# Kernel tuning notes

Measured on AMD Instinct MI355X. Metric: run time of the kernel, lower is better.

## Reference

```python
import jax, jax.numpy as jnp
import numpy as np

B, G, D, N_HEADS, FFN, L = 16, 2048, 256, 8, 1024, 4
HEAD_DIM = D // N_HEADS
EPS_LN = 1e-5
MASK_TOKEN = -10.0
REE_BASE = 100.0


def setup_inputs() -> dict:
    key = jax.random.key(0)
    ks = jax.random.split(key, 20)
    s = 0.02
    inp = {
        'x': jax.random.normal(ks[0], (B, G), jnp.float32),
        'gene_emb': jax.random.normal(ks[1], (G, D), jnp.float32) * s,
        'inv_freq': (1.0 / REE_BASE ** (jnp.arange(0, D, 2, dtype=jnp.float32) / D)),
        'Wq': jax.random.normal(ks[2], (L, D, D), jnp.float32) * s,
        'bq': jnp.zeros((L, D), jnp.float32),
        'Wk': jax.random.normal(ks[3], (L, D, D), jnp.float32) * s,
        'bk': jnp.zeros((L, D), jnp.float32),
        'Wv': jax.random.normal(ks[4], (L, D, D), jnp.float32) * s,
        'bv': jnp.zeros((L, D), jnp.float32),
        'ln1_g': jnp.ones((L, D), jnp.float32),
        'ln1_b': jnp.zeros((L, D), jnp.float32),
        'ln2_g': jnp.ones((L, D), jnp.float32),
        'ln2_b': jnp.zeros((L, D), jnp.float32),
        'WU': jax.random.normal(ks[5], (L, D, FFN), jnp.float32) * s,
        'bU': jnp.zeros((L, FFN), jnp.float32),
        'WV': jax.random.normal(ks[6], (L, FFN, D), jnp.float32) * s,
        'bV': jnp.zeros((L, D), jnp.float32),
        'Wout': jax.random.normal(ks[7], (D, 1), jnp.float32) * s,
        'bout': jnp.zeros((1,), jnp.float32),
    }
    return inp


def layernorm(x, g, b):
    m = x.mean(-1, keepdims=True)
    v = ((x - m) ** 2).mean(-1, keepdims=True)
    return (x - m) / jnp.sqrt(v + EPS_LN) * g + b


def causal_linear_attention(q, k, v):
    # q, k already feature-mapped ('sqr'); shapes [B, S, H, dh]
    b, s, h, dh = q.shape
    qs, ks_, vs = (jnp.moveaxis(t, 1, 0) for t in (q, k, v))  # [S,B,H,dh]
    num0 = jnp.zeros((b, h, dh, dh), q.dtype)
    den0 = jnp.zeros((b, h, dh), q.dtype)

    def step(carry, qkv):
        num_s, den_s = carry
        qt, kt, vt = qkv
        num_s = num_s + jnp.einsum('bhf,bhd->bhfd', kt, vt)
        den_s = den_s + kt
        num = jnp.einsum('bhf,bhfd->bhd', qt, num_s)
        den = jnp.einsum('bhf,bhf->bh', qt, den_s)
        return (num_s, den_s), num / (den[..., None] + 1e-16)

    _, out = jax.lax.scan(step, (num0, den0), (qs, ks_, vs))  # [S,B,H,dh]
    return jnp.moveaxis(out, 0, 1).reshape(b, s, h * dh)


def reference(x, gene_emb, inv_freq, Wq, bq, Wk, bk, Wv, bv,
              ln1_g, ln1_b, ln2_g, ln2_b, WU, bU, WV, bV, Wout, bout):
    b, g = x.shape
    # Rotary Expression Embedding
    freqs = x[..., None] * inv_freq  # [B,G,D/2]
    emb = jnp.concatenate([jnp.sin(freqs), jnp.cos(freqs)], axis=-1)  # [B,G,D]
    emb = jnp.where((x == MASK_TOKEN)[..., None], 0.0, emb)
    h = gene_emb[None] + emb  # [B,G,D]

    for l in range(Wq.shape[0]):
        hn = layernorm(h, ln1_g[l], ln1_b[l])  # pre-LN (on_gptln=True)
        q = (hn @ Wq[l] + bq[l]).reshape(b, g, N_HEADS, HEAD_DIM) ** 2
        k = (hn @ Wk[l] + bk[l]).reshape(b, g, N_HEADS, HEAD_DIM) ** 2
        v = (hn @ Wv[l] + bv[l]).reshape(b, g, N_HEADS, HEAD_DIM)
        h = h + causal_linear_attention(q, k, v)
        hn2 = layernorm(h, ln2_g[l], ln2_b[l])
        h = h + jax.nn.gelu(hn2 @ WU[l] + bU[l], approximate=False) @ WV[l] + bV[l]
    return (h @ Wout + bout).squeeze(-1)  # [B,G]
```

## Files before the change

kernel.cpp:

```cpp
#include <hip/hip_runtime.h>
#include <math.h>


#define GG 2048
#define DD 256
#define NROWS 32768
#define NC 32
#define CS 64

typedef __attribute__((ext_vector_type(8))) short bf16x8;
typedef __attribute__((ext_vector_type(4))) float f32x4;

__device__ __forceinline__ short f2bf(float f) {
  union { float f; unsigned u; } v; v.f = f;
  unsigned r = v.u + 0x7FFFu + ((v.u >> 16) & 1u);
  return (short)(r >> 16);
}
__device__ __forceinline__ float bf2f(short s) {
  union { unsigned u; float f; } v; v.u = ((unsigned)(unsigned short)s) << 16;
  return v.f;
}
__device__ __forceinline__ void gld16(const short* g, short* l) {
  __builtin_amdgcn_global_load_lds(
      (const __attribute__((address_space(1))) void*)g,
      (__attribute__((address_space(3))) void*)l, 16, 0, 0);
}
__device__ __forceinline__ float fast_gelu(float x) {
  float y = 1.595769122f * (x + 0.044715f * x * x * x);
  return x / (1.0f + __expf(-y));
}

__global__ __launch_bounds__(256) void embed_kernel(
    const float* __restrict__ x, const float* __restrict__ ge,
    const float* __restrict__ invf, float* __restrict__ h) {
  int bg = blockIdx.x * 4 + (threadIdx.x >> 6);
  int g = bg & (GG - 1);
  int lane = threadIdx.x & 63;
  float xv = x[bg];
  int d = lane * 4;
  float4 e;
  if (lane < 32) {
    float4 f = *(const float4*)&invf[d];
    e.x = sinf(xv * f.x); e.y = sinf(xv * f.y);
    e.z = sinf(xv * f.z); e.w = sinf(xv * f.w);
  } else {
    float4 f = *(const float4*)&invf[d - 128];
    e.x = cosf(xv * f.x); e.y = cosf(xv * f.y);
    e.z = cosf(xv * f.z); e.w = cosf(xv * f.w);
  }
  if (xv == -10.0f) { e.x = 0.f; e.y = 0.f; e.z = 0.f; e.w = 0.f; }
  float4 gv = *(const float4*)&ge[(size_t)g * DD + d];
  float4 o; o.x = gv.x + e.x; o.y = gv.y + e.y; o.z = gv.z + e.z; o.w = gv.w + e.w;
  *(float4*)&h[(size_t)bg * DD + d] = o;
}

__global__ __launch_bounds__(256) void ln_tiled(
    const float* __restrict__ h, const float* __restrict__ gamma,
    const float* __restrict__ beta, short* __restrict__ outT) {
  __shared__ float mean_s[32], rstd_s[32];
  __shared__ float gls[256], bls[256];
  int r0 = blockIdx.x * 32;
  int tid = threadIdx.x;
  gls[tid] = gamma[tid]; bls[tid] = beta[tid];
  {
    int row = tid >> 3, seg = tid & 7;
    const float4* hp = (const float4*)(h + (size_t)(r0 + row) * DD + seg * 32);
    float s = 0.f, s2 = 0.f;
#pragma unroll
    for (int i = 0; i < 8; ++i) {
      float4 v = hp[i];
      s += v.x + v.y + v.z + v.w;
      s2 += v.x * v.x + v.y * v.y + v.z * v.z + v.w * v.w;
    }
    s += __shfl_xor(s, 1); s += __shfl_xor(s, 2); s += __shfl_xor(s, 4);
    s2 += __shfl_xor(s2, 1); s2 += __shfl_xor(s2, 2); s2 += __shfl_xor(s2, 4);
    if (seg == 0) {
      float mn = s * (1.0f / 256.0f);
      mean_s[row] = mn;
      rstd_s[row] = rsqrtf(s2 * (1.0f / 256.0f) - mn * mn + 1e-5f);
    }
  }
  __syncthreads();
  int row = tid & 31, kc8 = (tid >> 5) & 3, half = tid >> 7;
  float mn = mean_s[row], rs = rstd_s[row];
  size_t hrow = (size_t)(r0 + row) * DD;
  int trow = (r0 & 127) + row;
  short* tb = outT + (size_t)(r0 >> 7) * 8 * 4096 + (kc8 * 128 + trow) * 8;
#pragma unroll
  for (int j = 0; j < 4; ++j) {
    int kb = half * 4 + j;
    int k0 = kb * 32 + kc8 * 8;
    float4 x0 = *(const float4*)&h[hrow + k0];
    float4 x1 = *(const float4*)&h[hrow + k0 + 4];
    float4 g0 = *(const float4*)&gls[k0], g1 = *(const float4*)&gls[k0 + 4];
    float4 b0 = *(const float4*)&bls[k0], b1 = *(const float4*)&bls[k0 + 4];
    bf16x8 aw;
    aw[0] = f2bf((x0.x - mn) * rs * g0.x + b0.x);
    aw[1] = f2bf((x0.y - mn) * rs * g0.y + b0.y);
    aw[2] = f2bf((x0.z - mn) * rs * g0.z + b0.z);
    aw[3] = f2bf((x0.w - mn) * rs * g0.w + b0.w);
    aw[4] = f2bf((x1.x - mn) * rs * g1.x + b1.x);
    aw[5] = f2bf((x1.y - mn) * rs * g1.y + b1.y);
    aw[6] = f2bf((x1.z - mn) * rs * g1.z + b1.z);
    aw[7] = f2bf((x1.w - mn) * rs * g1.w + b1.w);
    *(bf16x8*)&tb[(size_t)kb * 4096] = aw;
  }
}

__global__ __launch_bounds__(256) void prep_weights(
    const float* __restrict__ Wq, const float* __restrict__ Wk,
    const float* __restrict__ Wv, const float* __restrict__ WU,
    const float* __restrict__ WV,
    short* __restrict__ TQ, short* __restrict__ TK, short* __restrict__ TV,
    short* __restrict__ TU, short* __restrict__ TVd) {
  int zz = blockIdx.z, l = blockIdx.y;
  const float* src; short* dst; int Kd, Nd;
  if (zz == 0) { src = Wq; dst = TQ; Kd = 256; Nd = 256; }
  else if (zz == 1) { src = Wk; dst = TK; Kd = 256; Nd = 256; }
  else if (zz == 2) { src = Wv; dst = TV; Kd = 256; Nd = 256; }
  else if (zz == 3) { src = WU; dst = TU; Kd = 256; Nd = 1024; }
  else { src = WV; dst = TVd; Kd = 1024; Nd = 256; }
  int tot = Kd * Nd;
  int e = blockIdx.x * 256 + threadIdx.x;
  if (e >= tot) return;
  int t = e >> 12;
  int cslot = (e >> 3) & 511;
  int elem = e & 7;
  int kc8 = cslot >> 7, rn = cslot & 127;
  int nKb = Kd >> 5;
  int nt = t / nKb, kb = t - nt * nKb;
  int n = nt * 128 + rn, k = kb * 32 + kc8 * 8 + elem;
  dst[(size_t)l * tot + e] = f2bf(src[(size_t)l * tot + (size_t)k * Nd + n]);
}

template <int K, int EPI>
__global__ __launch_bounds__(256) void gemm_t(
    const short* __restrict__ A, const short* __restrict__ B0,
    const short* __restrict__ B1, const short* __restrict__ B2,
    const float* __restrict__ bias0, const float* __restrict__ bias1,
    const float* __restrict__ bias2,
    short* __restrict__ o0, short* __restrict__ o1, short* __restrict__ o2,
    float* __restrict__ outf, int N) {
  __shared__ __align__(16) short L[24576];
  constexpr int nIter = K / 32;
  int z = blockIdx.z;
  const short* Bt = (z == 0) ? B0 : (z == 1) ? B1 : B2;
  const float* bias = (z == 0) ? bias0 : (z == 1) ? bias1 : bias2;
  short* outz = (z == 0) ? o0 : (z == 1) ? o1 : o2;
  int m0 = blockIdx.x * 128, n0 = blockIdx.y * 128;
  int tid = threadIdx.x;
  int lane = tid & 63, w = tid >> 6;
  int q = lane >> 4, r = lane & 15;
  int wm = (w >> 1) * 64, wn = (w & 1) * 64;
  const short* At = A + (size_t)blockIdx.x * nIter * 4096;
  const short* Btl = Bt + (size_t)blockIdx.y * nIter * 4096;
  f32x4 vzero = {0.f, 0.f, 0.f, 0.f};
  f32x4 acc[4][4];
#pragma unroll
  for (int i = 0; i < 4; ++i)
#pragma unroll
    for (int j = 0; j < 4; ++j) acc[i][j] = vzero;

  int c0 = tid * 8, c1 = (tid + 256) * 8;
#pragma unroll
  for (int g = 0; g < 3; ++g) {
    gld16(At + g * 4096 + c0, &L[g * 4096 + c0]);
    gld16(At + g * 4096 + c1, &L[g * 4096 + c1]);
    gld16(Btl + g * 4096 + c0, &L[12288 + g * 4096 + c0]);
    gld16(Btl + g * 4096 + c1, &L[12288 + g * 4096 + c1]);
  }

  int abase = (q * 128 + wm + r) * 8;
  int bbase = (q * 128 + wn + r) * 8;

#pragma unroll
  for (int gi = 0; gi < nIter; ++gi) {
    const int rem = nIter - 1 - gi;
    if (rem >= 2)      __builtin_amdgcn_s_waitcnt(0x0f78);
    else if (rem == 1) __builtin_amdgcn_s_waitcnt(0x0f74);
    else               __builtin_amdgcn_s_waitcnt(0x0f70);
    __builtin_amdgcn_s_barrier();
    const int cur = gi % 3;
    const short* Asc = &L[cur * 4096];
    const short* Bsc = &L[12288 + cur * 4096];
    bf16x8 af[4], bfr[4];
#pragma unroll
    for (int mt = 0; mt < 4; ++mt)
      af[mt] = *(const bf16x8*)&Asc[abase + mt * 16 * 8];
#pragma unroll
    for (int nt = 0; nt < 4; ++nt)
      bfr[nt] = *(const bf16x8*)&Bsc[bbase + nt * 16 * 8];
#pragma unroll
    for (int mt = 0; mt < 4; ++mt)
#pragma unroll
      for (int nt = 0; nt < 4; ++nt)
        acc[mt][nt] = __builtin_amdgcn_mfma_f32_16x16x32_bf16(bfr[nt], af[mt], acc[mt][nt], 0, 0, 0);
    __builtin_amdgcn_s_waitcnt(0xc07f);
    __builtin_amdgcn_s_barrier();
    if (gi + 3 < nIter) {
      size_t kn = (size_t)(gi + 3) * 4096;
      gld16(At + kn + c0, &L[cur * 4096 + c0]);
      gld16(At + kn + c1, &L[cur * 4096 + c1]);
      gld16(Btl + kn + c0, &L[12288 + cur * 4096 + c0]);
      gld16(Btl + kn + c1, &L[12288 + cur * 4096 + c1]);
    }
  }

  float4 bias4[4];
#pragma unroll
  for (int nt = 0; nt < 4; ++nt) bias4[nt] = *(const float4*)&bias[n0 + wn + nt * 16 + q * 4];

  if (EPI == 0) {
    short* T = L;
#pragma unroll
    for (int mt = 0; mt < 4; ++mt) {
      int ml = wm + mt * 16 + r;
#pragma unroll
      for (int nt = 0; nt < 4; ++nt) {
        f32x4 v = acc[mt][nt];
        v[0] += bias4[nt].x; v[1] += bias4[nt].y; v[2] += bias4[nt].z; v[3] += bias4[nt].w;
        if (z < 2) { v[0] *= v[0]; v[1] *= v[1]; v[2] *= v[2]; v[3] *= v[3]; }
        short4 pk; pk.x = f2bf(v[0]); pk.y = f2bf(v[1]); pk.z = f2bf(v[2]); pk.w = f2bf(v[3]);
        *(short4*)&T[ml * 132 + wn + nt * 16 + q * 4] = pk;
      }
    }
    __syncthreads();
#pragma unroll
    for (int t2 = 0; t2 < 2; ++t2) {
      int task = tid + t2 * 256;
      int row = task & 127, hl = task >> 7;
      size_t obase = ((size_t)((n0 >> 5) + hl) * NROWS + m0 + row) * 32;
#pragma unroll
      for (int j = 0; j < 4; ++j)
        *(bf16x8*)&outz[obase + j * 8] = *(const bf16x8*)&T[row * 132 + hl * 32 + j * 8];
    }
  } else if (EPI == 1) {
#pragma unroll
    for (int mt = 0; mt < 4; ++mt) {
      int ml = wm + mt * 16 + r;
#pragma unroll
      for (int nt = 0; nt < 4; ++nt) {
        f32x4 v = acc[mt][nt];
        v[0] += bias4[nt].x; v[1] += bias4[nt].y; v[2] += bias4[nt].z; v[3] += bias4[nt].w;
#pragma unroll
        for (int e = 0; e < 4; ++e) v[e] = fast_gelu(v[e]);
        short4 o; o.x = f2bf(v[0]); o.y = f2bf(v[1]); o.z = f2bf(v[2]); o.w = f2bf(v[3]);
        int n = n0 + wn + nt * 16 + q * 4;
        size_t ti = ((size_t)blockIdx.x * (N >> 5) + (n >> 5)) * 4096 +
                    (size_t)(((n >> 3) & 3) << 10) + (ml << 3) + (n & 7);
        *(short4*)&outz[ti] = o;
      }
    }
  } else {
    float* TF = (float*)L;
#pragma unroll
    for (int half = 0; half < 2; ++half) {
      __syncthreads();
      if ((w & 1) == half) {
#pragma unroll
        for (int mt = 0; mt < 4; ++mt) {
          int ml = wm + mt * 16 + r;
#pragma unroll
          for (int nt = 0; nt < 4; ++nt) {
            f32x4 v = acc[mt][nt];
            v[0] += bias4[nt].x; v[1] += bias4[nt].y; v[2] += bias4[nt].z; v[3] += bias4[nt].w;
            *(f32x4*)&TF[ml * 68 + nt * 16 + q * 4] = v;
          }
        }
      }
      __syncthreads();
      int row = tid >> 1, col = (tid & 1) * 32;
      size_t hoff = (size_t)(m0 + row) * N + n0 + half * 64 + col;
#pragma unroll
      for (int j = 0; j < 8; ++j) {
        float4 add = *(const float4*)&TF[row * 68 + col + j * 4];
        float4 cur4 = *(float4*)&outf[hoff + j * 4];
        cur4.x += add.x; cur4.y += add.y; cur4.z += add.z; cur4.w += add.w;
        *(float4*)&outf[hoff + j * 4] = cur4;
      }
    }
  }
}

__global__ __launch_bounds__(256) void attn_chunk_kv(
    const short* __restrict__ Kb, const short* __restrict__ Vb,
    float* __restrict__ St, float* __restrict__ Zc) {
  __shared__ short Kt[4][32 * 72];
  __shared__ short Vt[4][32 * 72];
  int wid = threadIdx.x >> 6;
  int blk = blockIdx.x * 4 + wid;
  int c = blk & (NC - 1), bh = blk >> 5;
  int b = bh >> 3, hh = bh & 7;
  int lane = threadIdx.x & 63, q = lane >> 4, r = lane & 15;
  size_t rowbase = ((size_t)hh * NROWS + b * GG + c * CS + lane) * 32;
#pragma unroll
  for (int j = 0; j < 4; ++j) {
    bf16x8 kv = *(const bf16x8*)&Kb[rowbase + j * 8];
    bf16x8 vv = *(const bf16x8*)&Vb[rowbase + j * 8];
#pragma unroll
    for (int e = 0; e < 8; ++e) {
      Kt[wid][(j * 8 + e) * 72 + lane] = kv[e];
      Vt[wid][(j * 8 + e) * 72 + lane] = vv[e];
    }
  }
  __syncthreads();
  f32x4 vzero = {0.f, 0.f, 0.f, 0.f};
  f32x4 acc[2][2];
#pragma unroll
  for (int i = 0; i < 2; ++i)
#pragma unroll
    for (int j = 0; j < 2; ++j) acc[i][j] = vzero;
#pragma unroll
  for (int ks = 0; ks < 2; ++ks) {
    bf16x8 afr[2], bfr[2];
#pragma unroll
    for (int mt = 0; mt < 2; ++mt) afr[mt] = *(const bf16x8*)&Kt[wid][(mt * 16 + r) * 72 + ks * 32 + q * 8];
#pragma unroll
    for (int nt = 0; nt < 2; ++nt) bfr[nt] = *(const bf16x8*)&Vt[wid][(nt * 16 + r) * 72 + ks * 32 + q * 8];
#pragma unroll
    for (int mt = 0; mt < 2; ++mt)
#pragma unroll
      for (int nt = 0; nt < 2; ++nt)
        acc[mt][nt] = __builtin_amdgcn_mfma_f32_16x16x32_bf16(afr[mt], bfr[nt], acc[mt][nt], 0, 0, 0);
  }
  float* stp = St + ((size_t)bh * NC + c) * 1024;
#pragma unroll
  for (int mt = 0; mt < 2; ++mt)
#pragma unroll
    for (int nt = 0; nt < 2; ++nt)
      *(f32x4*)&stp[(nt * 16 + r) * 32 + mt * 16 + q * 4] = acc[mt][nt];
  if (lane < 32) {
    float s = 0.f;
#pragma unroll
    for (int j = 0; j < 8; ++j) {
      bf16x8 kr = *(const bf16x8*)&Kt[wid][lane * 72 + j * 8];
#pragma unroll
      for (int e = 0; e < 8; ++e) s += bf2f(kr[e]);
    }
    Zc[((size_t)bh * NC + c) * 32 + lane] = s;
  }
}

__global__ __launch_bounds__(1024) void attn_prefix(float* __restrict__ St, float* __restrict__ Zc) {
  int bh = blockIdx.x, i = threadIdx.x;
  float run = 0.f;
  float* p = St + (size_t)bh * NC * 1024 + i;
#pragma unroll
  for (int c = 0; c < NC; ++c) { float t = p[(size_t)c * 1024]; p[(size_t)c * 1024] = run; run += t; }
  if (i < 32) {
    float rz = 0.f;
    float* pz = Zc + (size_t)bh * NC * 32 + i;
#pragma unroll
    for (int c = 0; c < NC; ++c) { float t = pz[c * 32]; pz[c * 32] = rz; rz += t; }
  }
}

__global__ __launch_bounds__(256) void attn_intra(
    const short* __restrict__ Qb, const short* __restrict__ Kb,
    const short* __restrict__ Vb, const float* __restrict__ St,
    const float* __restrict__ Zc, float* __restrict__ h) {
  __shared__ short P[4][64 * 72];
  __shared__ short Vt[4][32 * 72];
  __shared__ float den[4][64];
  int wid = threadIdx.x >> 6;
  int blk = blockIdx.x * 4 + wid;
  int c = blk & (NC - 1), bh = blk >> 5;
  int b = bh >> 3, hh = bh & 7;
  int lane = threadIdx.x & 63, q = lane >> 4, r = lane & 15;
  size_t hrow0 = (size_t)b * GG + c * CS;
  size_t qrow0 = (size_t)hh * NROWS + b * GG + c * CS;

  const float* zp = Zc + ((size_t)bh * NC + c) * 32;
  float qz = 0.f;
  {
    size_t qoff = (qrow0 + lane) * 32;
#pragma unroll
    for (int j = 0; j < 4; ++j) {
      bf16x8 qv = *(const bf16x8*)&Qb[qoff + j * 8];
#pragma unroll
      for (int e = 0; e < 8; ++e) qz += bf2f(qv[e]) * zp[j * 8 + e];
    }
  }
  den[wid][lane] = qz;

  {
    size_t voff = (qrow0 + lane) * 32;
#pragma unroll
    for (int j = 0; j < 4; ++j) {
      bf16x8 vv = *(const bf16x8*)&Vb[voff + j * 8];
#pragma unroll
      for (int e = 0; e < 8; ++e) Vt[wid][(j * 8 + e) * 72 + lane] = vv[e];
    }
  }

  bf16x8 ak[4], bqf[4];
#pragma unroll
  for (int t4 = 0; t4 < 4; ++t4) {
    ak[t4]  = *(const bf16x8*)&Kb[(qrow0 + t4 * 16 + r) * 32 + q * 8];
    bqf[t4] = *(const bf16x8*)&Qb[(qrow0 + t4 * 16 + r) * 32 + q * 8];
  }
  f32x4 vzero = {0.f, 0.f, 0.f, 0.f};
  f32x4 pacc[4][4];
#pragma unroll
  for (int mt = 0; mt < 4; ++mt)
#pragma unroll
    for (int nt = 0; nt < 4; ++nt)
      pacc[mt][nt] = __builtin_amdgcn_mfma_f32_16x16x32_bf16(ak[mt], bqf[nt], vzero, 0, 0, 0);

  float rs[4] = {0.f, 0.f, 0.f, 0.f};
#pragma unroll
  for (int nt = 0; nt < 4; ++nt) {
    int t = nt * 16 + r;
#pragma unroll
    for (int mt = 0; mt < 4; ++mt) {
      short4 pk;
#pragma unroll
      for (int rr = 0; rr < 4; ++rr) {
        int s = mt * 16 + q * 4 + rr;
        float pv = (s <= t) ? pacc[mt][nt][rr] : 0.f;
        rs[nt] += pv;
        ((short*)&pk)[rr] = f2bf(pv);
      }
      *(short4*)&P[wid][t * 72 + mt * 16 + q * 4] = pk;
    }
  }
#pragma unroll
  for (int nt = 0; nt < 4; ++nt) {
    rs[nt] += __shfl_xor(rs[nt], 16);
    rs[nt] += __shfl_xor(rs[nt], 32);
  }
  __syncthreads();
  if (lane < 16) {
#pragma unroll
    for (int nt = 0; nt < 4; ++nt) den[wid][nt * 16 + lane] += rs[nt];
  }
  __syncthreads();

  f32x4 oacc[4][2];
#pragma unroll
  for (int mt = 0; mt < 4; ++mt)
#pragma unroll
    for (int nt2 = 0; nt2 < 2; ++nt2) oacc[mt][nt2] = vzero;
  const float* stp = St + ((size_t)bh * NC + c) * 1024;
#pragma unroll
  for (int nt2 = 0; nt2 < 2; ++nt2) {
    float4 s0 = *(const float4*)&stp[(nt2 * 16 + r) * 32 + q * 8];
    float4 s1 = *(const float4*)&stp[(nt2 * 16 + r) * 32 + q * 8 + 4];
    bf16x8 bs;
    bs[0] = f2bf(s0.x); bs[1] = f2bf(s0.y); bs[2] = f2bf(s0.z); bs[3] = f2bf(s0.w);
    bs[4] = f2bf(s1.x); bs[5] = f2bf(s1.y); bs[6] = f2bf(s1.z); bs[7] = f2bf(s1.w);
#pragma unroll
    for (int mt = 0; mt < 4; ++mt)
      oacc[mt][nt2] = __builtin_amdgcn_mfma_f32_16x16x32_bf16(bqf[mt], bs, oacc[mt][nt2], 0, 0, 0);
  }
#pragma unroll
  for (int ks = 0; ks < 2; ++ks) {
    bf16x8 ap[4];
#pragma unroll
    for (int mt = 0; mt < 4; ++mt)
      ap[mt] = *(const bf16x8*)&P[wid][(mt * 16 + r) * 72 + ks * 32 + q * 8];
#pragma unroll
    for (int nt2 = 0; nt2 < 2; ++nt2) {
      bf16x8 bv_ = *(const bf16x8*)&Vt[wid][(nt2 * 16 + r) * 72 + ks * 32 + q * 8];
#pragma unroll
      for (int mt = 0; mt < 4; ++mt)
        oacc[mt][nt2] = __builtin_amdgcn_mfma_f32_16x16x32_bf16(ap[mt], bv_, oacc[mt][nt2], 0, 0, 0);
    }
  }

#pragma unroll
  for (int mt = 0; mt < 4; ++mt) {
#pragma unroll
    for (int rr = 0; rr < 4; ++rr) {
      int t = mt * 16 + q * 4 + rr;
      float inv = 1.0f / (den[wid][t] + 1e-16f);
#pragma unroll
      for (int nt2 = 0; nt2 < 2; ++nt2) {
        int d = nt2 * 16 + r;
        size_t off = (hrow0 + t) * DD + hh * 32 + d;
        h[off] += oacc[mt][nt2][rr] * inv;
      }
    }
  }
}

__global__ __launch_bounds__(256) void out_proj(
    const float* __restrict__ h, const float* __restrict__ Wout,
    const float* __restrict__ bout, float* __restrict__ out) {
  int row = blockIdx.x * 4 + (threadIdx.x >> 6);
  int lane = threadIdx.x & 63;
  float4 a = *(const float4*)&h[(size_t)row * DD + lane * 4];
  float4 w = *(const float4*)&Wout[lane * 4];
  float s = a.x * w.x + a.y * w.y + a.z * w.z + a.w * w.w;
#pragma unroll
  for (int o = 1; o < 64; o <<= 1) s += __shfl_xor(s, o);
  if (lane == 0) out[row] = s + bout[0];
}

extern "C" void kernel_launch(void* const* d_in, const int* in_sizes, int n_in,
                              void* d_out, int out_size, void* d_ws, size_t ws_size,
                              hipStream_t stream) {
  const float* x    = (const float*)d_in[0];
  const float* ge   = (const float*)d_in[1];
  const float* invf = (const float*)d_in[2];
  const float* Wq   = (const float*)d_in[3];
  const float* bq   = (const float*)d_in[4];
  const float* Wk   = (const float*)d_in[5];
  const float* bk   = (const float*)d_in[6];
  const float* Wv   = (const float*)d_in[7];
  const float* bv   = (const float*)d_in[8];
  const float* ln1g = (const float*)d_in[9];
  const float* ln1b = (const float*)d_in[10];
  const float* ln2g = (const float*)d_in[11];
  const float* ln2b = (const float*)d_in[12];
  const float* WU   = (const float*)d_in[13];
  const float* bU   = (const float*)d_in[14];
  const float* WV   = (const float*)d_in[15];
  const float* bV   = (const float*)d_in[16];
  const float* Wout = (const float*)d_in[17];
  const float* bout = (const float*)d_in[18];
  float* out = (float*)d_out;

  char* ws = (char*)d_ws;
  float* h   = (float*)(ws + 0);
  short* hn  = (short*)(ws + 33554432);
  char*  R   = ws + 50331648;
  short* qb  = (short*)(R + 0);
  short* kb  = (short*)(R + 16777216);
  short* vb  = (short*)(R + 33554432);
  float* St  = (float*)(R + 50331648);
  float* Zc  = (float*)(R + 67108864);
  short* mid = (short*)(R + 0);
  char*  WT  = R + 67633152;
  short* TQ  = (short*)(WT + 0);
  short* TK  = (short*)(WT + 524288);
  short* TVq = (short*)(WT + 1048576);
  short* TU  = (short*)(WT + 1572864);
  short* TVd = (short*)(WT + 3670016);

  prep_weights<<<dim3(1024, 4, 5), 256, 0, stream>>>(Wq, Wk, Wv, WU, WV, TQ, TK, TVq, TU, TVd);
  embed_kernel<<<NROWS / 4, 256, 0, stream>>>(x, ge, invf, h);

  for (int l = 0; l < 4; ++l) {
    ln_tiled<<<NROWS / 32, 256, 0, stream>>>(h, ln1g + l * 256, ln1b + l * 256, hn);
    gemm_t<256, 0><<<dim3(256, 2, 3), 256, 0, stream>>>(
        hn, TQ + l * 65536, TK + l * 65536, TVq + l * 65536,
        bq + l * 256, bk + l * 256, bv + l * 256,
        qb, kb, vb, nullptr, 256);
    attn_chunk_kv<<<1024, 256, 0, stream>>>(kb, vb, St, Zc);
    attn_prefix<<<128, 1024, 0, stream>>>(St, Zc);
    attn_intra<<<1024, 256, 0, stream>>>(qb, kb, vb, St, Zc, h);
    ln_tiled<<<NROWS / 32, 256, 0, stream>>>(h, ln2g + l * 256, ln2b + l * 256, hn);
    gemm_t<256, 1><<<dim3(256, 8, 1), 256, 0, stream>>>(
        hn, TU + l * 262144, nullptr, nullptr,
        bU + l * 1024, nullptr, nullptr,
        mid, nullptr, nullptr, nullptr, 1024);
    gemm_t<1024, 2><<<dim3(256, 2, 1), 256, 0, stream>>>(
        mid, TVd + l * 262144, nullptr, nullptr,
        bV + l * 256, nullptr, nullptr,
        nullptr, nullptr, nullptr, h, 256);
  }
  out_proj<<<NROWS / 4, 256, 0, stream>>>(h, Wout, bout, out);
}
```

Before: 762.5 us.

## Fuse FFN up-projection, GELU and down-projection into one kernel

Replaces the two FFN GEMM launches with a single kernel. Each block of 64 rows computes 128-column chunks of the GELU intermediate into shared memory, then immediately multiplies each chunk by the matching slice of the down-projection weights, accumulating into registers. This avoids writing and re-reading the 32768x1024 bf16 intermediate through global memory and saves one launch. The cost is that the down-projection weight loads are not double-buffered and sit behind barriers, the per-block M tile is smaller, and register pressure is high (16 accumulators plus the first GEMM's state), which may reduce occupancy.

After: 833.1 us. +9.3%, slower.

```diff
diff --git a/kernel.cpp b/kernel.cpp
--- a/kernel.cpp
+++ b/kernel.cpp
@@ -133,16 +133,14 @@
   dst[(size_t)l * tot + e] = f2bf(src[(size_t)l * tot + (size_t)k * Nd + n]);
 }
 
-template <int K, int EPI>
-__global__ __launch_bounds__(256) void gemm_t(
+__global__ __launch_bounds__(256) void gemm_qkv(
     const short* __restrict__ A, const short* __restrict__ B0,
     const short* __restrict__ B1, const short* __restrict__ B2,
     const float* __restrict__ bias0, const float* __restrict__ bias1,
     const float* __restrict__ bias2,
-    short* __restrict__ o0, short* __restrict__ o1, short* __restrict__ o2,
-    float* __restrict__ outf, int N) {
+    short* __restrict__ o0, short* __restrict__ o1, short* __restrict__ o2) {
   __shared__ __align__(16) short L[24576];
-  constexpr int nIter = K / 32;
+  constexpr int nIter = 8;
   int z = blockIdx.z;
   const short* Bt = (z == 0) ? B0 : (z == 1) ? B1 : B2;
   const float* bias = (z == 0) ? bias0 : (z == 1) ? bias1 : bias2;
@@ -169,7 +167,6 @@
     gld16(Btl + g * 4096 + c0, &L[12288 + g * 4096 + c0]);
     gld16(Btl + g * 4096 + c1, &L[12288 + g * 4096 + c1]);
   }
-
   int abase = (q * 128 + wm + r) * 8;
   int bbase = (q * 128 + wn + r) * 8;
 
@@ -209,75 +206,158 @@
   float4 bias4[4];
 #pragma unroll
   for (int nt = 0; nt < 4; ++nt) bias4[nt] = *(const float4*)&bias[n0 + wn + nt * 16 + q * 4];
-
-  if (EPI == 0) {
-    short* T = L;
-#pragma unroll
-    for (int mt = 0; mt < 4; ++mt) {
-      int ml = wm + mt * 16 + r;
+  short* T = L;
+#pragma unroll
+  for (int mt = 0; mt < 4; ++mt) {
+    int ml = wm + mt * 16 + r;
+#pragma unroll
+    for (int nt = 0; nt < 4; ++nt) {
+      f32x4 v = acc[mt][nt];
+      v[0] += bias4[nt].x; v[1] += bias4[nt].y; v[2] += bias4[nt].z; v[3] += bias4[nt].w;
+      if (z < 2) { v[0] *= v[0]; v[1] *= v[1]; v[2] *= v[2]; v[3] *= v[3]; }
+      short4 pk; pk.x = f2bf(v[0]); pk.y = f2bf(v[1]); pk.z = f2bf(v[2]); pk.w = f2bf(v[3]);
+      *(short4*)&T[ml * 132 + wn + nt * 16 + q * 4] = pk;
+    }
+  }
+  __syncthreads();
+#pragma unroll
+  for (int t2 = 0; t2 < 2; ++t2) {
+    int task = tid + t2 * 256;
+    int row = task & 127, hl = task >> 7;
+    size_t obase = ((size_t)((n0 >> 5) + hl) * NROWS + m0 + row) * 32;
+#pragma unroll
+    for (int j = 0; j < 4; ++j)
+      *(bf16x8*)&outz[obase + j * 8] = *(const bf16x8*)&T[row * 132 + hl * 32 + j * 8];
+  }
+}
+
+__global__ __launch_bounds__(256, 2) void ffn_fused(
+    const short* __restrict__ hnT, const short* __restrict__ TU,
+    const short* __restrict__ TVd,
+    const float* __restrict__ bU, const float* __restrict__ bV,
+    float* __restrict__ h) {
+  __shared__ __align__(16) short S[21248];
+  short* MID = &S[12288];
+  int tid = threadIdx.x;
+  int lane = tid & 63, w = tid >> 6;
+  int q = lane >> 4, r = lane & 15;
+  int m0 = blockIdx.x * 64;
+  int wm1 = (w >> 1) * 32, wn1 = (w & 1) * 64;
+  int wm2 = w * 16;
+  const short* Abase = hnT + (size_t)(m0 >> 7) * 32768 +
+                       ((tid >> 6) * 128 + (m0 & 127) + (tid & 63)) * 8;
+  int c0 = tid * 8, c1 = (tid + 256) * 8;
+
+  f32x4 vzero = {0.f, 0.f, 0.f, 0.f};
+  f32x4 acc2[16];
+#pragma unroll
+  for (int i = 0; i < 16; ++i) acc2[i] = vzero;
+
+  int ab1 = (q * 64 + wm1 + r) * 8;
+  int bb1 = (q * 128 + wn1 + r) * 8;
+  int ab2 = (wm2 + r) * 136 + q * 8;
+
+  for (int f = 0; f < 8; ++f) {
+    const short* Ub = TU + (size_t)f * 8 * 4096;
+#pragma unroll
+    for (int g = 0; g < 2; ++g) {
+      gld16(Abase + g * 4096, &S[g * 2048 + tid * 8]);
+      gld16(Ub + g * 4096 + c0, &S[4096 + g * 4096 + c0]);
+      gld16(Ub + g * 4096 + c1, &S[4096 + g * 4096 + c1]);
+    }
+    f32x4 acc1[2][4];
+#pragma unroll
+    for (int i = 0; i < 2; ++i)
+#pragma unroll
+      for (int j = 0; j < 4; ++j) acc1[i][j] = vzero;
+#pragma unroll
+    for (int gi = 0; gi < 8; ++gi) {
+      if (gi < 7) __builtin_amdgcn_s_waitcnt(0x0f73);
+      else        __builtin_amdgcn_s_waitcnt(0x0f70);
+      __builtin_amdgcn_s_barrier();
+      const int cur = gi & 1;
+      const short* Asc = &S[cur * 2048];
+      const short* Bsc = &S[4096 + cur * 4096];
+      bf16x8 af[2], bfr[4];
+#pragma unroll
+      for (int mt = 0; mt < 2; ++mt)
+        af[mt] = *(const bf16x8*)&Asc[ab1 + mt * 16 * 8];
+#pragma unroll
+      for (int nt = 0; nt < 4; ++nt)
+        bfr[nt] = *(const bf16x8*)&Bsc[bb1 + nt * 16 * 8];
+#pragma unroll
+      for (int mt = 0; mt < 2; ++mt)
+#pragma unroll
+        for (int nt = 0; nt < 4; ++nt)
+          acc1[mt][nt] = __builtin_amdgcn_mfma_f32_16x16x32_bf16(bfr[nt], af[mt], acc1[mt][nt], 0, 0, 0);
+      __builtin_amdgcn_s_waitcnt(0xc07f);
+      __builtin_amdgcn_s_barrier();
+      if (gi + 2 < 8) {
+        size_t kn = (size_t)(gi + 2) * 4096;
+        gld16(Abase + kn, &S[cur * 2048 + tid * 8]);
+        gld16(Ub + kn + c0, &S[4096 + cur * 4096 + c0]);
+        gld16(Ub + kn + c1, &S[4096 + cur * 4096 + c1]);
+      }
+    }
+#pragma unroll
+    for (int mt = 0; mt < 2; ++mt) {
+      int ml = wm1 + mt * 16 + r;
 #pragma unroll
       for (int nt = 0; nt < 4; ++nt) {
-        f32x4 v = acc[mt][nt];
-        v[0] += bias4[nt].x; v[1] += bias4[nt].y; v[2] += bias4[nt].z; v[3] += bias4[nt].w;
-        if (z < 2) { v[0] *= v[0]; v[1] *= v[1]; v[2] *= v[2]; v[3] *= v[3]; }
+        int fl = wn1 + nt * 16 + q * 4;
+        float4 bu4 = *(const float4*)&bU[f * 128 + fl];
+        f32x4 v = acc1[mt][nt];
+        v[0] = fast_gelu(v[0] + bu4.x); v[1] = fast_gelu(v[1] + bu4.y);
+        v[2] = fast_gelu(v[2] + bu4.z); v[3] = fast_gelu(v[3] + bu4.w);
         short4 pk; pk.x = f2bf(v[0]); pk.y = f2bf(v[1]); pk.z = f2bf(v[2]); pk.w = f2bf(v[3]);
-        *(short4*)&T[ml * 132 + wn + nt * 16 + q * 4] = pk;
+        *(short4*)&MID[ml * 136 + fl] = pk;
       }
     }
+#pragma unroll
+    for (int kb2 = 0; kb2 < 4; ++kb2) {
+      const short* Vb0 = TVd + (size_t)(4 * f + kb2) * 4096;
+      const short* Vb1 = Vb0 + (size_t)32 * 4096;
+      gld16(Vb0 + c0, &S[4096 + c0]);
+      gld16(Vb0 + c1, &S[4096 + c1]);
+      gld16(Vb1 + c0, &S[8192 + c0]);
+      gld16(Vb1 + c1, &S[8192 + c1]);
+      __builtin_amdgcn_s_waitcnt(0x0070);
+      __builtin_amdgcn_s_barrier();
+      bf16x8 af1 = *(const bf16x8*)&MID[ab2 + kb2 * 32];
+#pragma unroll
+      for (int nt = 0; nt < 16; ++nt) {
+        int tile = nt >> 3, nl = nt & 7;
+        bf16x8 bfr = *(const bf16x8*)&S[4096 + tile * 4096 + (q * 128 + nl * 16 + r) * 8];
+        acc2[nt] = __builtin_amdgcn_mfma_f32_16x16x32_bf16(bfr, af1, acc2[nt], 0, 0, 0);
+      }
+      __builtin_amdgcn_s_waitcnt(0xc07f);
+      __builtin_amdgcn_s_barrier();
+    }
+  }
+
+  float* TF = (float*)S;
+  float4 bv4[16];
+#pragma unroll
+  for (int nt = 0; nt < 16; ++nt) bv4[nt] = *(const float4*)&bV[nt * 16 + q * 4];
+#pragma unroll
+  for (int half = 0; half < 2; ++half) {
     __syncthreads();
 #pragma unroll
-    for (int t2 = 0; t2 < 2; ++t2) {
-      int task = tid + t2 * 256;
-      int row = task & 127, hl = task >> 7;
-      size_t obase = ((size_t)((n0 >> 5) + hl) * NROWS + m0 + row) * 32;
-#pragma unroll
-      for (int j = 0; j < 4; ++j)
-        *(bf16x8*)&outz[obase + j * 8] = *(const bf16x8*)&T[row * 132 + hl * 32 + j * 8];
-    }
-  } else if (EPI == 1) {
-#pragma unroll
-    for (int mt = 0; mt < 4; ++mt) {
-      int ml = wm + mt * 16 + r;
-#pragma unroll
-      for (int nt = 0; nt < 4; ++nt) {
-        f32x4 v = acc[mt][nt];
-        v[0] += bias4[nt].x; v[1] += bias4[nt].y; v[2] += bias4[nt].z; v[3] += bias4[nt].w;
-#pragma unroll
-        for (int e = 0; e < 4; ++e) v[e] = fast_gelu(v[e]);
-        short4 o; o.x = f2bf(v[0]); o.y = f2bf(v[1]); o.z = f2bf(v[2]); o.w = f2bf(v[3]);
-        int n = n0 + wn + nt * 16 + q * 4;
-        size_t ti = ((size_t)blockIdx.x * (N >> 5) + (n >> 5)) * 4096 +
-                    (size_t)(((n >> 3) & 3) << 10) + (ml << 3) + (n & 7);
-        *(short4*)&outz[ti] = o;
-      }
-    }
-  } else {
-    float* TF = (float*)L;
-#pragma unroll
-    for (int half = 0; half < 2; ++half) {
-      __syncthreads();
-      if ((w & 1) == half) {
-#pragma unroll
-        for (int mt = 0; mt < 4; ++mt) {
-          int ml = wm + mt * 16 + r;
-#pragma unroll
-          for (int nt = 0; nt < 4; ++nt) {
-            f32x4 v = acc[mt][nt];
-            v[0] += bias4[nt].x; v[1] += bias4[nt].y; v[2] += bias4[nt].z; v[3] += bias4[nt].w;
-            *(f32x4*)&TF[ml * 68 + nt * 16 + q * 4] = v;
-          }
-        }
-      }
-      __syncthreads();
-      int row = tid >> 1, col = (tid & 1) * 32;
-      size_t hoff = (size_t)(m0 + row) * N + n0 + half * 64 + col;
-#pragma unroll
-      for (int j = 0; j < 8; ++j) {
-        float4 add = *(const float4*)&TF[row * 68 + col + j * 4];
-        float4 cur4 = *(float4*)&outf[hoff + j * 4];
-        cur4.x += add.x; cur4.y += add.y; cur4.z += add.z; cur4.w += add.w;
-        *(float4*)&outf[hoff + j * 4] = cur4;
-      }
+    for (int nt8 = 0; nt8 < 8; ++nt8) {
+      int nt = half * 8 + nt8;
+      f32x4 v = acc2[nt];
+      v[0] += bv4[nt].x; v[1] += bv4[nt].y; v[2] += bv4[nt].z; v[3] += bv4[nt].w;
+      *(f32x4*)&TF[(wm2 + r) * 132 + nt8 * 16 + q * 4] = v;
+    }
+    __syncthreads();
+    int row = tid >> 2, seg = tid & 3;
+    size_t hoff = (size_t)(m0 + row) * DD + half * 128 + seg * 32;
+#pragma unroll
+    for (int j = 0; j < 8; ++j) {
+      float4 add = *(const float4*)&TF[row * 132 + seg * 32 + j * 4];
+      float4 cur4 = *(float4*)&h[hoff + j * 4];
+      cur4.x += add.x; cur4.y += add.y; cur4.z += add.z; cur4.w += add.w;
+      *(float4*)&h[hoff + j * 4] = cur4;
     }
   }
 }
@@ -382,7 +462,6 @@
     }
   }
   den[wid][lane] = qz;
-
   {
     size_t voff = (qrow0 + lane) * 32;
 #pragma unroll
@@ -392,7 +471,6 @@
       for (int e = 0; e < 8; ++e) Vt[wid][(j * 8 + e) * 72 + lane] = vv[e];
     }
   }
-
   bf16x8 ak[4], bqf[4];
 #pragma unroll
   for (int t4 = 0; t4 < 4; ++t4) {
@@ -467,7 +545,6 @@
         oacc[mt][nt2] = __builtin_amdgcn_mfma_f32_16x16x32_bf16(ap[mt], bv_, oacc[mt][nt2], 0, 0, 0);
     }
   }
-
 #pragma unroll
   for (int mt = 0; mt < 4; ++mt) {
 #pragma unroll
@@ -530,7 +607,6 @@
   short* vb  = (short*)(R + 33554432);
   float* St  = (float*)(R + 50331648);
   float* Zc  = (float*)(R + 67108864);
-  short* mid = (short*)(R + 0);
   char*  WT  = R + 67633152;
   short* TQ  = (short*)(WT + 0);
   short* TK  = (short*)(WT + 524288);
@@ -543,22 +619,16 @@
 
   for (int l = 0; l < 4; ++l) {
     ln_tiled<<<NROWS / 32, 256, 0, stream>>>(h, ln1g + l * 256, ln1b + l * 256, hn);
-    gemm_t<256, 0><<<dim3(256, 2, 3), 256, 0, stream>>>(
+    gemm_qkv<<<dim3(256, 2, 3), 256, 0, stream>>>(
         hn, TQ + l * 65536, TK + l * 65536, TVq + l * 65536,
-        bq + l * 256, bk + l * 256, bv + l * 256,
-        qb, kb, vb, nullptr, 256);
+        bq + l * 256, bk + l * 256, bv + l * 256, qb, kb, vb);
     attn_chunk_kv<<<1024, 256, 0, stream>>>(kb, vb, St, Zc);
     attn_prefix<<<128, 1024, 0, stream>>>(St, Zc);
     attn_intra<<<1024, 256, 0, stream>>>(qb, kb, vb, St, Zc, h);
     ln_tiled<<<NROWS / 32, 256, 0, stream>>>(h, ln2g + l * 256, ln2b + l * 256, hn);
-    gemm_t<256, 1><<<dim3(256, 8, 1), 256, 0, stream>>>(
-        hn, TU + l * 262144, nullptr, nullptr,
-        bU + l * 1024, nullptr, nullptr,
-        mid, nullptr, nullptr, nullptr, 1024);
-    gemm_t<1024, 2><<<dim3(256, 2, 1), 256, 0, stream>>>(
-        mid, TVd + l * 262144, nullptr, nullptr,
-        bV + l * 256, nullptr, nullptr,
-        nullptr, nullptr, nullptr, h, 256);
+    ffn_fused<<<NROWS / 64, 256, 0, stream>>>(
+        hn, TU + l * 262144, TVd + l * 262144,
+        bU + l * 1024, bV + l * 256, h);
   }
   out_proj<<<NROWS / 4, 256, 0, stream>>>(h, Wout, bout, out);
 }
```
